# Performance work log

Measured on AMD Instinct MI355X. Metric: run time of the kernel, lower is better.

Reference implementation:

```python
import jax, jax.numpy as jnp
import numpy as np

VOXEL = 128
N_PTS = VOXEL ** 3  # 2,097,152
C_FEAT = 14
T_HASH = 4194304


def _hash_index(coords, table_size):
    # Instant-NGP style spatial hash: elementwise prime multiply, xor-reduce, mod T.
    # uint32 arithmetic emulates the wrap-around semantics of the integer hash.
    primes = jnp.array([1, 2654435761, 805459861], dtype=jnp.uint32)
    h = coords.astype(jnp.uint32) * primes  # [N, 3]
    return ((h[:, 0] ^ h[:, 1]) ^ h[:, 2]) % jnp.uint32(table_size)  # [N]


def _quat_to_rotmat(q):
    # q: [N, 4] normalized, (r, x, y, z) convention (standard 3DGS)
    r, x, y, z = q[:, 0], q[:, 1], q[:, 2], q[:, 3]
    R = jnp.stack([
        1 - 2 * (y * y + z * z), 2 * (x * y - r * z), 2 * (x * z + r * y),
        2 * (x * y + r * z), 1 - 2 * (x * x + z * z), 2 * (y * z - r * x),
        2 * (x * z - r * y), 2 * (y * z + r * x), 1 - 2 * (x * x + y * y),
    ], axis=-1)
    return R.reshape(-1, 3, 3)


def setup_inputs() -> dict:
    key = jax.random.key(0)
    k1, k2, k3 = jax.random.split(key, 3)
    coordinates = jax.random.randint(k1, (N_PTS, 3), 0, VOXEL, dtype=jnp.int32)
    hash_table = jax.random.normal(k2, (C_FEAT, T_HASH), dtype=jnp.float32)
    camera_center = jax.random.normal(k3, (3,), dtype=jnp.float32)
    far = jnp.ones((1,), dtype=jnp.float32)
    return {"coordinates": coordinates, "hash_table": hash_table,
            "camera_center": camera_center, "far": far, "voxel_size": VOXEL}


def reference(coordinates, hash_table, camera_center, far, voxel_size):
    far_s = far[0]
    vs = jnp.float32(voxel_size)

    # hash_query: [C, N] gather from hash table
    idx = _hash_index(coordinates, hash_table.shape[1])
    gf = hash_table[:, idx]  # [14, N]

    # compute_voxel_center: [N, 3]
    voxel_center = (coordinates.astype(jnp.float32) / vs * 2 * far_s
                    - far_s + camera_center[None, :] + far_s / vs)

    # delta means: normalize over ALL elements (torch.mean/std on full tensor, unbiased std)
    dm = gf[0:3].T  # [N, 3]
    dm = (dm - jnp.mean(dm)) / jnp.std(dm, ddof=1) * 2 * far_s / vs / 6.0
    means = dm + voxel_center  # [N, 3]

    # covariance from scaling + rotation (standard 3DGS)
    scales = jax.nn.sigmoid(gf[7:10].T) * 2 * far_s / vs  # [N, 3]
    q = gf[3:7].T
    q = q / jnp.linalg.norm(q, axis=-1, keepdims=True)
    R = _quat_to_rotmat(q)                       # [N, 3, 3]
    L = R * scales[:, None, :]                   # L = R @ diag(s)
    covariances = jnp.einsum('nij,nkj->nik', L, L)  # [N, 3, 3]

    harmonics = gf[10:13].T[:, :, None]          # [N, 3, 1] (raw features)
    opacities = jax.nn.sigmoid(gf[13] - 4.0)     # [N]

    n = coordinates.shape[0]
    return (means[None], covariances[None], harmonics[None], opacities[None])
```

## Files before the change

kernel.cpp:

```cpp
#include <hip/hip_runtime.h>
#include <math.h>

#define N_PTS (128*128*128)
#define T_HASH 4194304
#define T_MASK (T_HASH - 1)
#define ENTRY_STRIDE 16

#define PA_BLOCKS  2048
#define PA_THREADS 256
#define PA_STRIDE  (PA_BLOCKS * PA_THREADS)
#define PA_ITERS   (N_PTS / PA_STRIDE)

__device__ __forceinline__ unsigned hash_idx(int x, int y, int z) {
    return ((unsigned)x ^ ((unsigned)y * 2654435761u)
                        ^ ((unsigned)z * 805459861u)) & T_MASK;
}

__global__ __launch_bounds__(256)
void transpose_kernel(const float* __restrict__ table, float* __restrict__ tt,
                      double* __restrict__ acc) {
    if (blockIdx.x == 0 && threadIdx.x < 2) acc[threadIdx.x] = 0.0;

    __shared__ float sh[16][258];
    const int t  = threadIdx.x;
    const int i0 = blockIdx.x * 256;

    #pragma unroll
    for (int k = 0; k < 7; ++k) {
        const int l    = t + k * 256;
        const int row  = l >> 7;
        const int col2 = (l & 127) * 2;
        const float2 v = *(const float2*)(table + (size_t)row * T_HASH + i0 + col2);
        *(float2*)&sh[row][col2] = v;
    }
    __syncthreads();

    const int c  = t & 3;
    const int r0 = c * 4;
    const int p0 = t >> 2;
    float4* dst = (float4*)(tt + (size_t)i0 * ENTRY_STRIDE);
    #pragma unroll
    for (int k = 0; k < 4; ++k) {
        const int p = p0 + k * 64;
        float vx = sh[r0 + 0][p];
        float vy = sh[r0 + 1][p];
        float vz = sh[r0 + 2][p];
        float vw = sh[r0 + 3][p];
        if (c == 3) { vz = 0.f; vw = 0.f; }
        dst[(size_t)p * 4 + c] = make_float4(vx, vy, vz, vw);
    }
}

__global__ __launch_bounds__(256)
void fused_main_kernel(const int*   __restrict__ coords,
                       const float* __restrict__ tt,
                       const float* __restrict__ far_p,
                       const int*   __restrict__ vs_p,
                       float*       __restrict__ out,
                       double*      __restrict__ acc) {
    const int base = blockIdx.x * PA_THREADS + threadIdx.x;

    int cx[PA_ITERS], cy[PA_ITERS], cz[PA_ITERS];
    #pragma unroll
    for (int it = 0; it < PA_ITERS; ++it) {
        const size_t b = (size_t)(base + it * PA_STRIDE) * 3;
        cx[it] = coords[b + 0];
        cy[it] = coords[b + 1];
        cz[it] = coords[b + 2];
    }

    float4 f0[PA_ITERS], f1[PA_ITERS], f2[PA_ITERS], f3[PA_ITERS];
    #pragma unroll
    for (int it = 0; it < PA_ITERS; ++it) {
        const unsigned idx = hash_idx(cx[it], cy[it], cz[it]);
        const float4* e = (const float4*)(tt + (size_t)idx * ENTRY_STRIDE);
        f0[it] = e[0]; f1[it] = e[1]; f2[it] = e[2]; f3[it] = e[3];
    }

    const float far_s = far_p[0];
    const float vs    = (float)vs_p[0];
    const float tfv   = 2.f * far_s / vs;

    float s = 0.f, ss = 0.f;
    #pragma unroll
    for (int it = 0; it < PA_ITERS; ++it) {
        const int i = base + it * PA_STRIDE;

        const float g0 = f0[it].x, g1 = f0[it].y, g2 = f0[it].z;
        out[(size_t)i * 3 + 0] = g0;
        out[(size_t)i * 3 + 1] = g1;
        out[(size_t)i * 3 + 2] = g2;
        s  += g0 + g1 + g2;
        ss += g0 * g0 + g1 * g1 + g2 * g2;

        float qr = f0[it].w, qx = f1[it].x, qy = f1[it].y, qz = f1[it].z;
        const float qinv = 1.f / sqrtf(qr * qr + qx * qx + qy * qy + qz * qz);
        qr *= qinv; qx *= qinv; qy *= qinv; qz *= qinv;

        float R[3][3];
        R[0][0] = 1.f - 2.f * (qy * qy + qz * qz);
        R[0][1] = 2.f * (qx * qy - qr * qz);
        R[0][2] = 2.f * (qx * qz + qr * qy);
        R[1][0] = 2.f * (qx * qy + qr * qz);
        R[1][1] = 1.f - 2.f * (qx * qx + qz * qz);
        R[1][2] = 2.f * (qy * qz - qr * qx);
        R[2][0] = 2.f * (qx * qz - qr * qy);
        R[2][1] = 2.f * (qy * qz + qr * qx);
        R[2][2] = 1.f - 2.f * (qx * qx + qy * qy);

        float sc[3];
        sc[0] = tfv / (1.f + expf(-f1[it].w));
        sc[1] = tfv / (1.f + expf(-f2[it].x));
        sc[2] = tfv / (1.f + expf(-f2[it].y));

        float L[3][3];
        #pragma unroll
        for (int r = 0; r < 3; ++r)
            #pragma unroll
            for (int j = 0; j < 3; ++j)
                L[r][j] = R[r][j] * sc[j];

        float* covp = out + (size_t)3 * N_PTS + (size_t)i * 9;
        #pragma unroll
        for (int r = 0; r < 3; ++r)
            #pragma unroll
            for (int col = 0; col < 3; ++col)
                covp[r * 3 + col] = L[r][0] * L[col][0]
                                  + L[r][1] * L[col][1]
                                  + L[r][2] * L[col][2];

        float* harp = out + (size_t)12 * N_PTS + (size_t)i * 3;
        harp[0] = f2[it].z;
        harp[1] = f2[it].w;
        harp[2] = f3[it].x;

        out[(size_t)15 * N_PTS + i] = 1.f / (1.f + expf(-(f3[it].y - 4.f)));
    }

    #pragma unroll
    for (int off = 32; off > 0; off >>= 1) {
        s  += __shfl_down(s, off, 64);
        ss += __shfl_down(ss, off, 64);
    }
    __shared__ float sh_s[4], sh_ss[4];
    const int lane = threadIdx.x & 63;
    const int wid  = threadIdx.x >> 6;
    if (lane == 0) { sh_s[wid] = s; sh_ss[wid] = ss; }
    __syncthreads();
    if (threadIdx.x == 0) {
        float ts = 0.f, tss = 0.f;
        for (int w = 0; w < 4; ++w) { ts += sh_s[w]; tss += sh_ss[w]; }
        atomicAdd(&acc[0], (double)ts);
        atomicAdd(&acc[1], (double)tss);
    }
}

__global__ __launch_bounds__(256)
void finalize_means_kernel(const int*    __restrict__ coords,
                           const float*  __restrict__ cam,
                           const float*  __restrict__ far_p,
                           const int*    __restrict__ vs_p,
                           const double* __restrict__ acc,
                           float*        __restrict__ out) {
    const double n      = 3.0 * (double)N_PTS;
    const double sum    = acc[0];
    const double sumsq  = acc[1];
    const float  mean   = (float)(sum / n);
    const float  inv_std= (float)(1.0 / sqrt((sumsq - sum * sum / n) / (n - 1.0)));

    const float far_s = far_p[0];
    const float vs    = (float)vs_p[0];
    const float a     = inv_std * (2.f * far_s / vs / 6.f);
    const float off_c = -far_s + far_s / vs;
    const float cam_t[3] = { cam[0], cam[1], cam[2] };

    const int base = blockIdx.x * PA_THREADS + threadIdx.x;
    #pragma unroll
    for (int it = 0; it < PA_ITERS; ++it) {
        const int i = base + it * PA_STRIDE;
        const size_t b = (size_t)i * 3;
        const int cc[3] = { coords[b + 0], coords[b + 1], coords[b + 2] };
        #pragma unroll
        for (int k = 0; k < 3; ++k) {
            const float vc = (float)cc[k] / vs * 2.f * far_s + off_c + cam_t[k];
            const float dm = out[b + k];
            out[b + k] = (dm - mean) * a + vc;
        }
    }
}

__global__ void reduce_kernel_o(const int* __restrict__ coords,
                                const float* __restrict__ table,
                                double* __restrict__ acc) {
    float s = 0.f, ss = 0.f;
    const int stride = gridDim.x * blockDim.x;
    for (int i = blockIdx.x * blockDim.x + threadIdx.x; i < N_PTS; i += stride) {
        const unsigned idx = hash_idx(coords[i*3], coords[i*3+1], coords[i*3+2]);
        float g0 = table[idx];
        float g1 = table[T_HASH + idx];
        float g2 = table[2 * T_HASH + idx];
        s  += g0 + g1 + g2;
        ss += g0 * g0 + g1 * g1 + g2 * g2;
    }
    #pragma unroll
    for (int off = 32; off > 0; off >>= 1) {
        s  += __shfl_down(s, off, 64);
        ss += __shfl_down(ss, off, 64);
    }
    __shared__ float sh_s[4], sh_ss[4];
    const int lane = threadIdx.x & 63;
    const int wid  = threadIdx.x >> 6;
    if (lane == 0) { sh_s[wid] = s; sh_ss[wid] = ss; }
    __syncthreads();
    if (threadIdx.x == 0) {
        float ts = 0.f, tss = 0.f;
        for (int w = 0; w < 4; ++w) { ts += sh_s[w]; tss += sh_ss[w]; }
        atomicAdd(&acc[0], (double)ts);
        atomicAdd(&acc[1], (double)tss);
    }
}

__global__ void main_kernel_o(const int* __restrict__ coords,
                              const float* __restrict__ tab,
                              const float* __restrict__ cam,
                              const float* __restrict__ far_p,
                              const int* __restrict__ vs_p,
                              const double* __restrict__ acc,
                              float* __restrict__ out) {
    const int i = blockIdx.x * blockDim.x + threadIdx.x;
    if (i >= N_PTS) return;

    const float far_s = far_p[0];
    const float vs    = (float)vs_p[0];

    const double n      = 3.0 * (double)N_PTS;
    const double sum    = acc[0];
    const double sumsq  = acc[1];
    const float mean    = (float)(sum / n);
    const float inv_std = (float)(1.0 / sqrt((sumsq - sum * sum / n) / (n - 1.0)));

    const int cx = coords[i * 3 + 0];
    const int cy = coords[i * 3 + 1];
    const int cz = coords[i * 3 + 2];
    const unsigned idx = hash_idx(cx, cy, cz);

    float g[14];
    #pragma unroll
    for (int j = 0; j < 14; ++j)
        g[j] = tab[(size_t)j * T_HASH + idx];

    const float two_far_over_vs = 2.f * far_s / vs;
    const float dm_scale = two_far_over_vs / 6.f;
    const float c_f[3] = { (float)cx, (float)cy, (float)cz };
    #pragma unroll
    for (int k = 0; k < 3; ++k) {
        const float vc = c_f[k] / vs * 2.f * far_s - far_s + cam[k] + far_s / vs;
        out[(size_t)i * 3 + k] = (g[k] - mean) * inv_std * dm_scale + vc;
    }

    float qr = g[3], qx = g[4], qy = g[5], qz = g[6];
    const float qinv = 1.f / sqrtf(qr * qr + qx * qx + qy * qy + qz * qz);
    qr *= qinv; qx *= qinv; qy *= qinv; qz *= qinv;

    float R[3][3];
    R[0][0] = 1.f - 2.f * (qy * qy + qz * qz);
    R[0][1] = 2.f * (qx * qy - qr * qz);
    R[0][2] = 2.f * (qx * qz + qr * qy);
    R[1][0] = 2.f * (qx * qy + qr * qz);
    R[1][1] = 1.f - 2.f * (qx * qx + qz * qz);
    R[1][2] = 2.f * (qy * qz - qr * qx);
    R[2][0] = 2.f * (qx * qz - qr * qy);
    R[2][1] = 2.f * (qy * qz + qr * qx);
    R[2][2] = 1.f - 2.f * (qx * qx + qy * qy);

    float sc[3];
    #pragma unroll
    for (int k = 0; k < 3; ++k)
        sc[k] = two_far_over_vs / (1.f + expf(-g[7 + k]));

    float* covp = out + (size_t)3 * N_PTS + (size_t)i * 9;
    #pragma unroll
    for (int r = 0; r < 3; ++r) {
        #pragma unroll
        for (int c = 0; c < 3; ++c) {
            float a = 0.f;
            #pragma unroll
            for (int j = 0; j < 3; ++j)
                a += (R[r][j] * sc[j]) * (R[c][j] * sc[j]);
            covp[r * 3 + c] = a;
        }
    }

    float* harp = out + (size_t)12 * N_PTS + (size_t)i * 3;
    #pragma unroll
    for (int k = 0; k < 3; ++k)
        harp[k] = g[10 + k];

    out[(size_t)15 * N_PTS + i] = 1.f / (1.f + expf(-(g[13] - 4.f)));
}

extern "C" void kernel_launch(void* const* d_in, const int* in_sizes, int n_in,
                              void* d_out, int out_size, void* d_ws, size_t ws_size,
                              hipStream_t stream) {
    const int*   coords = (const int*)d_in[0];
    const float* table  = (const float*)d_in[1];
    const float* cam    = (const float*)d_in[2];
    const float* far_p  = (const float*)d_in[3];
    const int*   vs_p   = (const int*)d_in[4];
    float*       out    = (float*)d_out;

    double* acc = (double*)d_ws;
    float*  tt  = (float*)((char*)d_ws + 256);

    const size_t need = 256 + (size_t)T_HASH * ENTRY_STRIDE * sizeof(float);

    if (ws_size >= need) {
        transpose_kernel<<<T_HASH / 256, 256, 0, stream>>>(table, tt, acc);
        fused_main_kernel<<<PA_BLOCKS, PA_THREADS, 0, stream>>>(coords, tt, far_p,
                                                                vs_p, out, acc);
        finalize_means_kernel<<<PA_BLOCKS, PA_THREADS, 0, stream>>>(coords, cam,
                                                                    far_p, vs_p,
                                                                    acc, out);
    } else {
        hipMemsetAsync(d_ws, 0, 2 * sizeof(double), stream);
        const int threads = 256;
        const int blocks  = (N_PTS + threads - 1) / threads;
        reduce_kernel_o<<<2048, 256, 0, stream>>>(coords, table, acc);
        main_kernel_o<<<blocks, threads, 0, stream>>>(coords, table, cam,
                                                      far_p, vs_p, acc, out);
    }
}
```

Baseline: 499.9 us.

## Merge means finalize into main kernel via grid-wide barrier, keep deltas in registers

Replaces the separate finalize kernel with a persistent-style kernel of 1024 blocks that, after accumulating the global sum and sum of squares, waits on an atomic grid barrier and then writes the normalized means directly from registers. Delta means and packed coordinates stay in registers, so the out buffer is no longer read back and coords are no longer re-read, and one launch is removed. Gathers are batched four at a time to limit register pressure. This relies on all 1024 blocks being co-resident (launch bounds of 4 per SM); if they are not, the spin loop only exits through its iteration guard, which would give wrong results. Having fewer blocks with more iterations each may also reduce memory-level parallelism.

```diff
diff --git a/kernel.cpp b/kernel.cpp
--- a/kernel.cpp
+++ b/kernel.cpp
@@ -1,15 +1,16 @@
 #include <hip/hip_runtime.h>
 #include <math.h>
+#include <string.h>
 
 #define N_PTS (128*128*128)
 #define T_HASH 4194304
 #define T_MASK (T_HASH - 1)
 #define ENTRY_STRIDE 16
 
-#define PA_BLOCKS  2048
-#define PA_THREADS 256
-#define PA_STRIDE  (PA_BLOCKS * PA_THREADS)
-#define PA_ITERS   (N_PTS / PA_STRIDE)
+#define CP_BLOCKS  1024
+#define CP_THREADS 256
+#define CP_STRIDE  (CP_BLOCKS * CP_THREADS)
+#define CP_ITERS   (N_PTS / CP_STRIDE)
 
 __device__ __forceinline__ unsigned hash_idx(int x, int y, int z) {
     return ((unsigned)x ^ ((unsigned)y * 2654435761u)
@@ -18,8 +19,10 @@
 
 __global__ __launch_bounds__(256)
 void transpose_kernel(const float* __restrict__ table, float* __restrict__ tt,
-                      double* __restrict__ acc) {
-    if (blockIdx.x == 0 && threadIdx.x < 2) acc[threadIdx.x] = 0.0;
+                      double* __restrict__ acc, unsigned* __restrict__ bar) {
+    if (blockIdx.x == 0 && threadIdx.x == 0) {
+        acc[0] = 0.0; acc[1] = 0.0; *bar = 0u;
+    }
 
     __shared__ float sh[16][258];
     const int t  = threadIdx.x;
@@ -51,90 +54,93 @@
     }
 }
 
-__global__ __launch_bounds__(256)
-void fused_main_kernel(const int*   __restrict__ coords,
+__global__ __launch_bounds__(256, 4)
+void fused_coop_kernel(const int*   __restrict__ coords,
                        const float* __restrict__ tt,
+                       const float* __restrict__ cam,
                        const float* __restrict__ far_p,
                        const int*   __restrict__ vs_p,
                        float*       __restrict__ out,
-                       double*      __restrict__ acc) {
-    const int base = blockIdx.x * PA_THREADS + threadIdx.x;
-
-    int cx[PA_ITERS], cy[PA_ITERS], cz[PA_ITERS];
-    #pragma unroll
-    for (int it = 0; it < PA_ITERS; ++it) {
-        const size_t b = (size_t)(base + it * PA_STRIDE) * 3;
-        cx[it] = coords[b + 0];
-        cy[it] = coords[b + 1];
-        cz[it] = coords[b + 2];
-    }
-
-    float4 f0[PA_ITERS], f1[PA_ITERS], f2[PA_ITERS], f3[PA_ITERS];
-    #pragma unroll
-    for (int it = 0; it < PA_ITERS; ++it) {
-        const unsigned idx = hash_idx(cx[it], cy[it], cz[it]);
-        const float4* e = (const float4*)(tt + (size_t)idx * ENTRY_STRIDE);
-        f0[it] = e[0]; f1[it] = e[1]; f2[it] = e[2]; f3[it] = e[3];
-    }
+                       double*      __restrict__ acc,
+                       unsigned*    __restrict__ bar) {
+    const int base = blockIdx.x * CP_THREADS + threadIdx.x;
 
     const float far_s = far_p[0];
     const float vs    = (float)vs_p[0];
     const float tfv   = 2.f * far_s / vs;
 
+    float dmx[CP_ITERS], dmy[CP_ITERS], dmz[CP_ITERS];
+    int   pk [CP_ITERS];
     float s = 0.f, ss = 0.f;
-    #pragma unroll
-    for (int it = 0; it < PA_ITERS; ++it) {
-        const int i = base + it * PA_STRIDE;
-
-        const float g0 = f0[it].x, g1 = f0[it].y, g2 = f0[it].z;
-        out[(size_t)i * 3 + 0] = g0;
-        out[(size_t)i * 3 + 1] = g1;
-        out[(size_t)i * 3 + 2] = g2;
-        s  += g0 + g1 + g2;
-        ss += g0 * g0 + g1 * g1 + g2 * g2;
-
-        float qr = f0[it].w, qx = f1[it].x, qy = f1[it].y, qz = f1[it].z;
-        const float qinv = 1.f / sqrtf(qr * qr + qx * qx + qy * qy + qz * qz);
-        qr *= qinv; qx *= qinv; qy *= qinv; qz *= qinv;
-
-        float R[3][3];
-        R[0][0] = 1.f - 2.f * (qy * qy + qz * qz);
-        R[0][1] = 2.f * (qx * qy - qr * qz);
-        R[0][2] = 2.f * (qx * qz + qr * qy);
-        R[1][0] = 2.f * (qx * qy + qr * qz);
-        R[1][1] = 1.f - 2.f * (qx * qx + qz * qz);
-        R[1][2] = 2.f * (qy * qz - qr * qx);
-        R[2][0] = 2.f * (qx * qz - qr * qy);
-        R[2][1] = 2.f * (qy * qz + qr * qx);
-        R[2][2] = 1.f - 2.f * (qx * qx + qy * qy);
-
-        float sc[3];
-        sc[0] = tfv / (1.f + expf(-f1[it].w));
-        sc[1] = tfv / (1.f + expf(-f2[it].x));
-        sc[2] = tfv / (1.f + expf(-f2[it].y));
-
-        float L[3][3];
+
+    #pragma unroll
+    for (int h = 0; h < CP_ITERS / 4; ++h) {
+        float4 f0[4], f1[4], f2[4], f3[4];
         #pragma unroll
-        for (int r = 0; r < 3; ++r)
+        for (int b = 0; b < 4; ++b) {
+            const int it = h * 4 + b;
+            const size_t cb = (size_t)(base + it * CP_STRIDE) * 3;
+            const int cx = coords[cb + 0];
+            const int cy = coords[cb + 1];
+            const int cz = coords[cb + 2];
+            pk[it] = cx | (cy << 7) | (cz << 14);
+            const unsigned idx = hash_idx(cx, cy, cz);
+            const float4* e = (const float4*)(tt + (size_t)idx * ENTRY_STRIDE);
+            f0[b] = e[0]; f1[b] = e[1]; f2[b] = e[2]; f3[b] = e[3];
+        }
+        #pragma unroll
+        for (int b = 0; b < 4; ++b) {
+            const int it = h * 4 + b;
+            const int i  = base + it * CP_STRIDE;
+
+            const float g0 = f0[b].x, g1 = f0[b].y, g2 = f0[b].z;
+            dmx[it] = g0; dmy[it] = g1; dmz[it] = g2;
+            s  += g0 + g1 + g2;
+            ss += g0 * g0 + g1 * g1 + g2 * g2;
+
+            float qr = f0[b].w, qx = f1[b].x, qy = f1[b].y, qz = f1[b].z;
+            const float qinv = 1.f / sqrtf(qr * qr + qx * qx + qy * qy + qz * qz);
+            qr *= qinv; qx *= qinv; qy *= qinv; qz *= qinv;
+
+            float R[3][3];
+            R[0][0] = 1.f - 2.f * (qy * qy + qz * qz);
+            R[0][1] = 2.f * (qx * qy - qr * qz);
+            R[0][2] = 2.f * (qx * qz + qr * qy);
+            R[1][0] = 2.f * (qx * qy + qr * qz);
+            R[1][1] = 1.f - 2.f * (qx * qx + qz * qz);
+            R[1][2] = 2.f * (qy * qz - qr * qx);
+            R[2][0] = 2.f * (qx * qz - qr * qy);
+            R[2][1] = 2.f * (qy * qz + qr * qx);
+            R[2][2] = 1.f - 2.f * (qx * qx + qy * qy);
+
+            float sc[3];
+            sc[0] = tfv / (1.f + expf(-f1[b].w));
+            sc[1] = tfv / (1.f + expf(-f2[b].x));
+            sc[2] = tfv / (1.f + expf(-f2[b].y));
+
+            float L[3][3];
             #pragma unroll
-            for (int j = 0; j < 3; ++j)
-                L[r][j] = R[r][j] * sc[j];
-
-        float* covp = out + (size_t)3 * N_PTS + (size_t)i * 9;
-        #pragma unroll
-        for (int r = 0; r < 3; ++r)
+            for (int r = 0; r < 3; ++r)
+                #pragma unroll
+                for (int j = 0; j < 3; ++j)
+                    L[r][j] = R[r][j] * sc[j];
+
+            float* covp = out + (size_t)3 * N_PTS + (size_t)i * 9;
             #pragma unroll
-            for (int col = 0; col < 3; ++col)
-                covp[r * 3 + col] = L[r][0] * L[col][0]
-                                  + L[r][1] * L[col][1]
-                                  + L[r][2] * L[col][2];
-
-        float* harp = out + (size_t)12 * N_PTS + (size_t)i * 3;
-        harp[0] = f2[it].z;
-        harp[1] = f2[it].w;
-        harp[2] = f3[it].x;
-
-        out[(size_t)15 * N_PTS + i] = 1.f / (1.f + expf(-(f3[it].y - 4.f)));
+            for (int r = 0; r < 3; ++r)
+                #pragma unroll
+                for (int col = 0; col < 3; ++col)
+                    covp[r * 3 + col] = L[r][0] * L[col][0]
+                                      + L[r][1] * L[col][1]
+                                      + L[r][2] * L[col][2];
+
+            float* harp = out + (size_t)12 * N_PTS + (size_t)i * 3;
+            harp[0] = f2[b].z;
+            harp[1] = f2[b].w;
+            harp[2] = f3[b].x;
+
+            out[(size_t)15 * N_PTS + i] = 1.f / (1.f + expf(-(f3[b].y - 4.f)));
+        }
     }
 
     #pragma unroll
@@ -152,40 +158,44 @@
         for (int w = 0; w < 4; ++w) { ts += sh_s[w]; tss += sh_ss[w]; }
         atomicAdd(&acc[0], (double)ts);
         atomicAdd(&acc[1], (double)tss);
-    }
-}
-
-__global__ __launch_bounds__(256)
-void finalize_means_kernel(const int*    __restrict__ coords,
-                           const float*  __restrict__ cam,
-                           const float*  __restrict__ far_p,
-                           const int*    __restrict__ vs_p,
-                           const double* __restrict__ acc,
-                           float*        __restrict__ out) {
+        __threadfence();
+        __hip_atomic_fetch_add(bar, 1u, __ATOMIC_RELEASE, __HIP_MEMORY_SCOPE_AGENT);
+        unsigned guard = 0;
+        while (__hip_atomic_load(bar, __ATOMIC_ACQUIRE, __HIP_MEMORY_SCOPE_AGENT)
+               < (unsigned)CP_BLOCKS) {
+            __builtin_amdgcn_s_sleep(32);
+            if (++guard > 500000u) break;
+        }
+    }
+    __syncthreads();
+
+    unsigned long long u0 = __hip_atomic_load((unsigned long long*)&acc[0],
+                                              __ATOMIC_RELAXED, __HIP_MEMORY_SCOPE_AGENT);
+    unsigned long long u1 = __hip_atomic_load((unsigned long long*)&acc[1],
+                                              __ATOMIC_RELAXED, __HIP_MEMORY_SCOPE_AGENT);
+    double sum, sumsq;
+    memcpy(&sum,   &u0, 8);
+    memcpy(&sumsq, &u1, 8);
+
     const double n      = 3.0 * (double)N_PTS;
-    const double sum    = acc[0];
-    const double sumsq  = acc[1];
     const float  mean   = (float)(sum / n);
     const float  inv_std= (float)(1.0 / sqrt((sumsq - sum * sum / n) / (n - 1.0)));
-
-    const float far_s = far_p[0];
-    const float vs    = (float)vs_p[0];
-    const float a     = inv_std * (2.f * far_s / vs / 6.f);
-    const float off_c = -far_s + far_s / vs;
-    const float cam_t[3] = { cam[0], cam[1], cam[2] };
-
-    const int base = blockIdx.x * PA_THREADS + threadIdx.x;
-    #pragma unroll
-    for (int it = 0; it < PA_ITERS; ++it) {
-        const int i = base + it * PA_STRIDE;
-        const size_t b = (size_t)i * 3;
-        const int cc[3] = { coords[b + 0], coords[b + 1], coords[b + 2] };
-        #pragma unroll
-        for (int k = 0; k < 3; ++k) {
-            const float vc = (float)cc[k] / vs * 2.f * far_s + off_c + cam_t[k];
-            const float dm = out[b + k];
-            out[b + k] = (dm - mean) * a + vc;
-        }
+    const float  a      = inv_std * (tfv / 6.f);
+    const float  off_c  = -far_s + far_s / vs;
+    const float  cam0 = cam[0], cam1 = cam[1], cam2 = cam[2];
+
+    #pragma unroll
+    for (int it = 0; it < CP_ITERS; ++it) {
+        const int i  = base + it * CP_STRIDE;
+        const int cx =  pk[it]        & 127;
+        const int cy = (pk[it] >> 7)  & 127;
+        const int cz =  pk[it] >> 14;
+        out[(size_t)i * 3 + 0] = (dmx[it] - mean) * a
+                               + ((float)cx / vs * 2.f * far_s + off_c + cam0);
+        out[(size_t)i * 3 + 1] = (dmy[it] - mean) * a
+                               + ((float)cy / vs * 2.f * far_s + off_c + cam1);
+        out[(size_t)i * 3 + 2] = (dmz[it] - mean) * a
+                               + ((float)cz / vs * 2.f * far_s + off_c + cam2);
     }
 }
 
@@ -309,18 +319,17 @@
     const int*   vs_p   = (const int*)d_in[4];
     float*       out    = (float*)d_out;
 
-    double* acc = (double*)d_ws;
-    float*  tt  = (float*)((char*)d_ws + 256);
+    double*   acc = (double*)d_ws;
+    unsigned* bar = (unsigned*)((char*)d_ws + 16);
+    float*    tt  = (float*)((char*)d_ws + 256);
 
     const size_t need = 256 + (size_t)T_HASH * ENTRY_STRIDE * sizeof(float);
 
     if (ws_size >= need) {
-        transpose_kernel<<<T_HASH / 256, 256, 0, stream>>>(table, tt, acc);
-        fused_main_kernel<<<PA_BLOCKS, PA_THREADS, 0, stream>>>(coords, tt, far_p,
-                                                                vs_p, out, acc);
-        finalize_means_kernel<<<PA_BLOCKS, PA_THREADS, 0, stream>>>(coords, cam,
-                                                                    far_p, vs_p,
-                                                                    acc, out);
+        transpose_kernel<<<T_HASH / 256, 256, 0, stream>>>(table, tt, acc, bar);
+        fused_coop_kernel<<<CP_BLOCKS, CP_THREADS, 0, stream>>>(coords, tt, cam,
+                                                                far_p, vs_p,
+                                                                out, acc, bar);
     } else {
         hipMemsetAsync(d_ws, 0, 2 * sizeof(double), stream);
         const int threads = 256;
```

After: 833.8 us. 1.67x slower.
